# Optimization experiments

Measured on AMD Instinct MI355X. Metric: run time of the kernel, lower is better.

Reference implementation:

```python
import jax, jax.numpy as jnp
import numpy as np

# Module hyperparameters (from init_kwargs)
NUM_NEURONS = 16384
BATCH = 2048  # processed sequentially, sharing neuron state
V_TH0 = 1.0
V_RESET = 0.0
TAU = 20.0
DT = 1.0
ETA = 0.1
NOISE_STD = 0.1
MIN_TH = 0.5
MAX_TH = 2.0
USE_ADAPTIVE = True
STOCHASTIC = True


def setup_inputs() -> dict:
    key = jax.random.key(0)
    k1, k2 = jax.random.split(key)
    input_current = jax.random.normal(k1, (BATCH, NUM_NEURONS), dtype=jnp.float32)
    # stochastic membrane noise, pre-sampled for determinism
    noise = NOISE_STD * jax.random.normal(k2, (BATCH, NUM_NEURONS), dtype=jnp.float32)
    if not STOCHASTIC:
        noise = jnp.zeros_like(noise)
    return {"input_current": input_current, "noise": noise}


def reference(input_current, noise):
    # Faithful to the torch wrapper: each batch row is fed through the SAME
    # LIFNeuronGroup sequentially, carrying membrane potential V and the
    # adaptive threshold V_th across rows -> lax.scan over the batch axis.
    n = input_current.shape[1]
    V0 = jnp.full((n,), V_RESET, dtype=jnp.float32)
    Vth0 = jnp.full((n,), V_TH0, dtype=jnp.float32)

    def step(carry, inp):
        V, Vth = carry
        I, nz = inp
        # leaky integration + noise injection (fused elementwise)
        V = V + (DT / TAU) * (I - V) + nz
        spikes = V >= Vth
        V = jnp.where(spikes, V_RESET, V)
        if USE_ADAPTIVE:
            Vth = jnp.clip(Vth + ETA * spikes.astype(jnp.float32), MIN_TH, MAX_TH)
        return (V, Vth), spikes.astype(jnp.float32)

    (_, _), out_spikes = jax.lax.scan(step, (V0, Vth0), (input_current, noise))
    return out_spikes  # [batch, num_neurons] binary float32
```

## Files before the change

### kernel.cpp

```cpp
#include <hip/hip_runtime.h>


constexpr int N = 16384;
constexpr int T = 2048;
constexpr int U = 4;
constexpr int C = T / U;
constexpr int R = 16;
constexpr int P = 14;

static_assert(C == 512 && R == 16 && P <= R - 2, "schedule geometry");

typedef float f4v __attribute__((ext_vector_type(4)));

__device__ __forceinline__ void dma16(const float* g, float* l) {
    __builtin_amdgcn_global_load_lds(
        (const __attribute__((address_space(1))) void*)g,
        (__attribute__((address_space(3))) void*)l, 16, 0, 0);
}

#define WAITV(K) asm volatile("s_waitcnt vmcnt(" #K ")" ::: "memory")

__global__
__attribute__((amdgpu_flat_work_group_size(64, 64)))
void TorchLIFNeuronGroup_85152021610615_kernel(const float* __restrict__ I,
                                               const float* __restrict__ Z,
                                               float* __restrict__ O) {
    #pragma clang fp contract(off)
    __shared__ __align__(16) float ring[R][2][U][64];
    __shared__ __align__(16) float sbuf[U][64];

    const int lane = threadIdx.x;
    const int g    = lane >> 4;
    const int c4   = (lane & 15) << 2;
    const size_t laneOff = (size_t)g * N + c4;

    const float* ipfx = I + (size_t)blockIdx.x * 64 + laneOff;
    const float* zpfx = Z + (size_t)blockIdx.x * 64 + laneOff;
    float*       opfx = O + (size_t)blockIdx.x * 64 + laneOff;

    float V   = 0.0f;
    float Vth = 1.0f;

    #pragma unroll
    for (int c = 0; c < P; ++c) {
        dma16(ipfx + (size_t)(c * U) * N, &ring[c][0][0][0]);
        dma16(zpfx + (size_t)(c * U) * N, &ring[c][1][0][0]);
    }

    int t = 0;

#define STAGE(d, K, PF)                                                       \
    {                                                                         \
        WAITV(K);                                                             \
        _Pragma("unroll")                                                     \
        for (int u = 0; u < U; ++u) {                                         \
            float Iv = ring[d][0][u][lane];                                   \
            float Zv = ring[d][1][u][lane];                                   \
            float dd = Iv - V;                                                \
            float v1 = V + 0.05f * dd;                            \
            float v2 = v1 + Zv;                                               \
            bool  s  = (v2 >= Vth);                                           \
            V = s ? 0.0f : v2;                                                \
            float nth = fminf(fmaxf(Vth + 0.1f, 0.5f), 2.0f);                 \
            Vth = s ? nth : Vth;                                              \
            sbuf[u][lane] = s ? 1.0f : 0.0f;                                  \
        }                                                                     \
        {                                                                     \
            f4v sv = *reinterpret_cast<const f4v*>(&sbuf[g][c4]);             \
            __builtin_nontemporal_store(                                      \
                sv, reinterpret_cast<f4v*>(opfx + (size_t)t * N));            \
        }                                                                     \
        if (PF) {                                                             \
            dma16(ipfx + (size_t)(t + P * U) * N,                             \
                  &ring[(d + P) & (R - 1)][0][0][0]);                         \
            dma16(zpfx + (size_t)(t + P * U) * N,                             \
                  &ring[(d + P) & (R - 1)][1][0][0]);                         \
        }                                                                     \
        __builtin_amdgcn_sched_barrier(0);                                    \
        t += U;                                                               \
    }

    STAGE(0, 26, 1)  STAGE(1, 27, 1)  STAGE(2, 28, 1)  STAGE(3, 29, 1)
    STAGE(4, 30, 1)  STAGE(5, 31, 1)  STAGE(6, 32, 1)  STAGE(7, 33, 1)
    STAGE(8, 34, 1)  STAGE(9, 35, 1)  STAGE(10, 36, 1) STAGE(11, 37, 1)
    STAGE(12, 38, 1) STAGE(13, 39, 1) STAGE(14, 39, 1) STAGE(15, 39, 1)

    for (int it = 1; it <= 30; ++it) {
        STAGE(0, 39, 1)  STAGE(1, 39, 1)  STAGE(2, 39, 1)  STAGE(3, 39, 1)
        STAGE(4, 39, 1)  STAGE(5, 39, 1)  STAGE(6, 39, 1)  STAGE(7, 39, 1)
        STAGE(8, 39, 1)  STAGE(9, 39, 1)  STAGE(10, 39, 1) STAGE(11, 39, 1)
        STAGE(12, 39, 1) STAGE(13, 39, 1) STAGE(14, 39, 1) STAGE(15, 39, 1)
    }

    STAGE(0, 39, 1)  STAGE(1, 39, 1)
    STAGE(2, 39, 0)  STAGE(3, 37, 0)  STAGE(4, 35, 0)  STAGE(5, 33, 0)
    STAGE(6, 31, 0)  STAGE(7, 29, 0)  STAGE(8, 27, 0)  STAGE(9, 25, 0)
    STAGE(10, 23, 0) STAGE(11, 21, 0) STAGE(12, 19, 0) STAGE(13, 17, 0)
    STAGE(14, 15, 0) STAGE(15, 13, 0)

#undef STAGE
}

extern "C" void kernel_launch(void* const* d_in, const int* in_sizes, int n_in,
                              void* d_out, int out_size, void* d_ws, size_t ws_size,
                              hipStream_t stream) {
    const float* input_current = (const float*)d_in[0];
    const float* noise         = (const float*)d_in[1];
    float* out                 = (float*)d_out;

    TorchLIFNeuronGroup_85152021610615_kernel<<<N / 64, 64, 0, stream>>>(
        input_current, noise, out);
}
```

Before: 313.1 us.

## Replace LDS DMA ring with register-held prefetch and skewed LDS transpose

Global loads now go into a 16-deep array of vector registers instead of using global_load_lds into an LDS ring with explicit vmcnt waits. Each stage transposes the next chunk through double-buffered LDS and stores the previous chunk's spikes one stage late, so LDS round-trips stay off the serial recurrence. waves_per_eu(1,1) lets the kernel use many registers. The aim is to cut per-stage latency on the dependent scan chain. The cost is much higher register pressure and waits the compiler now inserts for itself, which may be more conservative than the hand-tuned vmcnt values.

```diff
diff --git a/kernel.cpp b/kernel.cpp
--- a/kernel.cpp
+++ b/kernel.cpp
@@ -5,29 +5,23 @@
 constexpr int T = 2048;
 constexpr int U = 4;
 constexpr int C = T / U;
-constexpr int R = 16;
-constexpr int P = 14;
+constexpr int P = 16;
+constexpr int NB = C / P;
 
-static_assert(C == 512 && R == 16 && P <= R - 2, "schedule geometry");
+static_assert(C == NB * P, "schedule geometry");
 
 typedef float f4v __attribute__((ext_vector_type(4)));
 
-__device__ __forceinline__ void dma16(const float* g, float* l) {
-    __builtin_amdgcn_global_load_lds(
-        (const __attribute__((address_space(1))) void*)g,
-        (__attribute__((address_space(3))) void*)l, 16, 0, 0);
-}
-
-#define WAITV(K) asm volatile("s_waitcnt vmcnt(" #K ")" ::: "memory")
-
 __global__
 __attribute__((amdgpu_flat_work_group_size(64, 64)))
+__attribute__((amdgpu_waves_per_eu(1, 1)))
 void TorchLIFNeuronGroup_85152021610615_kernel(const float* __restrict__ I,
                                                const float* __restrict__ Z,
                                                float* __restrict__ O) {
     #pragma clang fp contract(off)
-    __shared__ __align__(16) float ring[R][2][U][64];
-    __shared__ __align__(16) float sbuf[U][64];
+    __shared__ __align__(16) float Ibuf[2][U][64];
+    __shared__ __align__(16) float Zbuf[2][U][64];
+    __shared__ __align__(16) float sbuf[2][U][64];
 
     const int lane = threadIdx.x;
     const int g    = lane >> 4;
@@ -40,22 +34,46 @@
 
     float V   = 0.0f;
     float Vth = 1.0f;
+    f4v   gI[P], gZ[P];
+    float cc[2][8];
 
     #pragma unroll
     for (int c = 0; c < P; ++c) {
-        dma16(ipfx + (size_t)(c * U) * N, &ring[c][0][0][0]);
-        dma16(zpfx + (size_t)(c * U) * N, &ring[c][1][0][0]);
+        gI[c] = __builtin_nontemporal_load(
+            reinterpret_cast<const f4v*>(ipfx + (size_t)(c * U) * N));
+        gZ[c] = __builtin_nontemporal_load(
+            reinterpret_cast<const f4v*>(zpfx + (size_t)(c * U) * N));
+    }
+    *reinterpret_cast<f4v*>(&Ibuf[0][0][0] + lane * 4) = gI[0];
+    *reinterpret_cast<f4v*>(&Zbuf[0][0][0] + lane * 4) = gZ[0];
+    #pragma unroll
+    for (int u = 0; u < U; ++u) {
+        cc[0][u]     = Ibuf[0][u][lane];
+        cc[0][4 + u] = Zbuf[0][u][lane];
     }
 
     int t = 0;
 
-#define STAGE(d, K, PF)                                                       \
+#define STAGE(j, CE, AB, PF)                                                  \
     {                                                                         \
-        WAITV(K);                                                             \
+        f4v sv{};                                                             \
+        if (CE) sv = *reinterpret_cast<const f4v*>(                           \
+                         &sbuf[((j) + 1) & 1][0][0] + lane * 4);              \
+        if (AB) {                                                             \
+            *reinterpret_cast<f4v*>(&Ibuf[((j) + 1) & 1][0][0] + lane * 4) =  \
+                gI[((j) + 1) & (P - 1)];                                      \
+            *reinterpret_cast<f4v*>(&Zbuf[((j) + 1) & 1][0][0] + lane * 4) =  \
+                gZ[((j) + 1) & (P - 1)];                                      \
+            _Pragma("unroll")                                                 \
+            for (int u = 0; u < U; ++u) {                                     \
+                cc[((j) + 1) & 1][u]     = Ibuf[((j) + 1) & 1][u][lane];      \
+                cc[((j) + 1) & 1][4 + u] = Zbuf[((j) + 1) & 1][u][lane];      \
+            }                                                                 \
+        }                                                                     \
         _Pragma("unroll")                                                     \
         for (int u = 0; u < U; ++u) {                                         \
-            float Iv = ring[d][0][u][lane];                                   \
-            float Zv = ring[d][1][u][lane];                                   \
+            float Iv = cc[(j) & 1][u];                                        \
+            float Zv = cc[(j) & 1][4 + u];                                    \
             float dd = Iv - V;                                                \
             float v1 = V + 0.05f * dd;                            \
             float v2 = v1 + Zv;                                               \
@@ -63,40 +81,49 @@
             V = s ? 0.0f : v2;                                                \
             float nth = fminf(fmaxf(Vth + 0.1f, 0.5f), 2.0f);                 \
             Vth = s ? nth : Vth;                                              \
-            sbuf[u][lane] = s ? 1.0f : 0.0f;                                  \
+            sbuf[(j) & 1][u][lane] = s ? 1.0f : 0.0f;                         \
         }                                                                     \
-        {                                                                     \
-            f4v sv = *reinterpret_cast<const f4v*>(&sbuf[g][c4]);             \
-            __builtin_nontemporal_store(                                      \
-                sv, reinterpret_cast<f4v*>(opfx + (size_t)t * N));            \
-        }                                                                     \
+        if (CE) __builtin_nontemporal_store(                                  \
+                    sv, reinterpret_cast<f4v*>(opfx + (size_t)(t - U) * N));  \
         if (PF) {                                                             \
-            dma16(ipfx + (size_t)(t + P * U) * N,                             \
-                  &ring[(d + P) & (R - 1)][0][0][0]);                         \
-            dma16(zpfx + (size_t)(t + P * U) * N,                             \
-                  &ring[(d + P) & (R - 1)][1][0][0]);                         \
+            gI[(j) & (P - 1)] = __builtin_nontemporal_load(                   \
+                reinterpret_cast<const f4v*>(ipfx + (size_t)(t + P * U) * N));\
+            gZ[(j) & (P - 1)] = __builtin_nontemporal_load(                   \
+                reinterpret_cast<const f4v*>(zpfx + (size_t)(t + P * U) * N));\
         }                                                                     \
         __builtin_amdgcn_sched_barrier(0);                                    \
         t += U;                                                               \
     }
 
-    STAGE(0, 26, 1)  STAGE(1, 27, 1)  STAGE(2, 28, 1)  STAGE(3, 29, 1)
-    STAGE(4, 30, 1)  STAGE(5, 31, 1)  STAGE(6, 32, 1)  STAGE(7, 33, 1)
-    STAGE(8, 34, 1)  STAGE(9, 35, 1)  STAGE(10, 36, 1) STAGE(11, 37, 1)
-    STAGE(12, 38, 1) STAGE(13, 39, 1) STAGE(14, 39, 1) STAGE(15, 39, 1)
+    STAGE(0, 0, 1, 1)   STAGE(1, 1, 1, 1)   STAGE(2, 1, 1, 1)
+    STAGE(3, 1, 1, 1)   STAGE(4, 1, 1, 1)   STAGE(5, 1, 1, 1)
+    STAGE(6, 1, 1, 1)   STAGE(7, 1, 1, 1)   STAGE(8, 1, 1, 1)
+    STAGE(9, 1, 1, 1)   STAGE(10, 1, 1, 1)  STAGE(11, 1, 1, 1)
+    STAGE(12, 1, 1, 1)  STAGE(13, 1, 1, 1)  STAGE(14, 1, 1, 1)
+    STAGE(15, 1, 1, 1)
 
-    for (int it = 1; it <= 30; ++it) {
-        STAGE(0, 39, 1)  STAGE(1, 39, 1)  STAGE(2, 39, 1)  STAGE(3, 39, 1)
-        STAGE(4, 39, 1)  STAGE(5, 39, 1)  STAGE(6, 39, 1)  STAGE(7, 39, 1)
-        STAGE(8, 39, 1)  STAGE(9, 39, 1)  STAGE(10, 39, 1) STAGE(11, 39, 1)
-        STAGE(12, 39, 1) STAGE(13, 39, 1) STAGE(14, 39, 1) STAGE(15, 39, 1)
+    #pragma clang loop unroll(disable)
+    for (int k = 1; k <= NB - 2; ++k) {
+        STAGE(0, 1, 1, 1)   STAGE(1, 1, 1, 1)   STAGE(2, 1, 1, 1)
+        STAGE(3, 1, 1, 1)   STAGE(4, 1, 1, 1)   STAGE(5, 1, 1, 1)
+        STAGE(6, 1, 1, 1)   STAGE(7, 1, 1, 1)   STAGE(8, 1, 1, 1)
+        STAGE(9, 1, 1, 1)   STAGE(10, 1, 1, 1)  STAGE(11, 1, 1, 1)
+        STAGE(12, 1, 1, 1)  STAGE(13, 1, 1, 1)  STAGE(14, 1, 1, 1)
+        STAGE(15, 1, 1, 1)
     }
 
-    STAGE(0, 39, 1)  STAGE(1, 39, 1)
-    STAGE(2, 39, 0)  STAGE(3, 37, 0)  STAGE(4, 35, 0)  STAGE(5, 33, 0)
-    STAGE(6, 31, 0)  STAGE(7, 29, 0)  STAGE(8, 27, 0)  STAGE(9, 25, 0)
-    STAGE(10, 23, 0) STAGE(11, 21, 0) STAGE(12, 19, 0) STAGE(13, 17, 0)
-    STAGE(14, 15, 0) STAGE(15, 13, 0)
+    STAGE(0, 1, 1, 0)   STAGE(1, 1, 1, 0)   STAGE(2, 1, 1, 0)
+    STAGE(3, 1, 1, 0)   STAGE(4, 1, 1, 0)   STAGE(5, 1, 1, 0)
+    STAGE(6, 1, 1, 0)   STAGE(7, 1, 1, 0)   STAGE(8, 1, 1, 0)
+    STAGE(9, 1, 1, 0)   STAGE(10, 1, 1, 0)  STAGE(11, 1, 1, 0)
+    STAGE(12, 1, 1, 0)  STAGE(13, 1, 1, 0)  STAGE(14, 1, 1, 0)
+    STAGE(15, 1, 0, 0)
+
+    {
+        f4v sv = *reinterpret_cast<const f4v*>(&sbuf[1][0][0] + lane * 4);
+        __builtin_nontemporal_store(
+            sv, reinterpret_cast<f4v*>(opfx + (size_t)(T - U) * N));
+    }
 
 #undef STAGE
 }
```

New measurement: 312.3 us. No clear change (-0.3%).
